# Kernel tuning notes

Hardware: AMD Instinct MI355X
Metric: run time of the kernel (lower is better)

Reference implementation:

```python
import jax, jax.numpy as jnp
import numpy as np

B, N, C, H = 4, 4096, 1024, 16
D = C // H


def setup_inputs() -> dict:
    key = jax.random.key(0)
    ks = jax.random.split(key, 15)
    s = 0.02
    f = lambda k, shp: jax.random.normal(k, shp, dtype=jnp.float32) * s
    return {
        "x": f(ks[0], (B, N, C)),
        "qkv_w": f(ks[1], (C, 3 * C)),
        "qkv_b": f(ks[2], (3 * C,)),
        "out_w": f(ks[3], (C, C)),
        "out_b": f(ks[4], (C,)),
        # NB: original code dynamically re-creates position_bias as (1, N, H, H)
        # because q/k/v are never transposed to (B,H,N,D); attention runs over heads.
        "pos_bias": f(ks[5], (1, N, H, H)),
        "conv_w": f(ks[6], (C, C)),
        "conv_b": f(ks[7], (C,)),
        "pw_w": f(ks[8], (C, C, 1)),   # Conv1d kernel_size=1: (out, in, k)
        "pw_b": f(ks[9], (C,)),
        "dw_w": f(ks[10], (C, 1, 3)),  # depthwise Conv1d groups=C: (out, in/groups=1, k)
        "dw_b": f(ks[11], (C,)),
        "tok_w": f(ks[12], (C, C)),
        "tok_b": f(ks[13], (C,)),
    }


def reference(x, qkv_w, qkv_b, out_w, out_b, pos_bias,
              conv_w, conv_b, pw_w, pw_b, dw_w, dw_b, tok_w, tok_b):
    b, n, c = x.shape
    h = pos_bias.shape[2]
    d = c // h
    scale = d ** (-0.5)

    # ---- attention branch (faithful to source: heads axis is attended over) ----
    qkv = (x @ qkv_w + qkv_b).reshape(b, n, h, 3 * d)
    q, k, v = jnp.split(qkv, 3, axis=-1)  # each (B, N, H, D)
    scores = jnp.einsum("bnhd,bngd->bnhg", q, k) * scale + pos_bias  # (B, N, H, H)
    attn_w = jax.nn.softmax(scores, axis=-1)
    attn = jnp.einsum("bnhg,bngd->bnhd", attn_w, v).reshape(b, n, c)
    attn = attn @ out_w + out_b

    # ---- convolutional branch ----
    xc = x @ conv_w + conv_b            # (B, N, C)
    xc = xc.transpose(0, 2, 1)          # (B, C, N)
    dn = ("NCH", "OIH", "NCH")
    xc = jax.lax.conv_general_dilated(xc, pw_w, (1,), [(0, 0)],
                                      dimension_numbers=dn) + pw_b[None, :, None]
    xc = jax.lax.conv_general_dilated(xc, dw_w, (1,), [(1, 1)],
                                      dimension_numbers=dn,
                                      feature_group_count=c) + dw_b[None, :, None]
    xc = xc.transpose(0, 2, 1) @ tok_w + tok_b  # (B, N, C)

    return attn + xc
```

## Files before the change

kernel.cpp:

```cpp
#include <hip/hip_runtime.h>
#include <hip/hip_bf16.h>


typedef __attribute__((ext_vector_type(8))) short sh8;
typedef __attribute__((ext_vector_type(4))) float f4;

__device__ __forceinline__ float bf2f(short s) {
  unsigned u = ((unsigned)(unsigned short)s) << 16;
  return __builtin_bit_cast(float, u);
}
__device__ __forceinline__ short f2bf(float f) {
  return __builtin_bit_cast(short, __float2bfloat16(f));
}
__device__ __forceinline__ void g2l16(const void* g, void* l) {
  __builtin_amdgcn_global_load_lds(
      (const __attribute__((address_space(1))) unsigned int*)g,
      (__attribute__((address_space(3))) unsigned int*)l, 16, 0, 0);
}

__global__ __launch_bounds__(256) void cvt_f32_bf16(
    const float* __restrict__ src, short* __restrict__ dst, int n8) {
  int i = blockIdx.x * 256 + threadIdx.x;
  if (i >= n8) return;
  float4 a = ((const float4*)src)[i * 2];
  float4 b = ((const float4*)src)[i * 2 + 1];
  sh8 o;
  o[0] = f2bf(a.x); o[1] = f2bf(a.y); o[2] = f2bf(a.z); o[3] = f2bf(a.w);
  o[4] = f2bf(b.x); o[5] = f2bf(b.y); o[6] = f2bf(b.z); o[7] = f2bf(b.w);
  ((sh8*)dst)[i] = o;
}

__global__ __launch_bounds__(256) void transpose_f32_bf16(
    const float* __restrict__ src, short* __restrict__ dst,
    int N, int ldd, int coff) {
  __shared__ float tile[32][33];
  int kb = blockIdx.y * 32, nb = blockIdx.x * 32;
  int tx = threadIdx.x, ty = threadIdx.y;
#pragma unroll
  for (int j = 0; j < 32; j += 8)
    tile[ty + j][tx] = src[(size_t)(kb + ty + j) * N + nb + tx];
  __syncthreads();
#pragma unroll
  for (int j = 0; j < 32; j += 8)
    dst[(size_t)(nb + ty + j) * ldd + coff + kb + tx] = f2bf(tile[tx][ty + j]);
}

__global__ __launch_bounds__(256) void prep_misc(
    const float* __restrict__ pw_w, const float* __restrict__ conv_b,
    const float* __restrict__ pw_b, const float* __restrict__ qkv_b,
    const float* __restrict__ out_b, const float* __restrict__ tok_b,
    const float* __restrict__ dw_w, const float* __restrict__ dw_b,
    float* __restrict__ bias4, float* __restrict__ bcat,
    float* __restrict__ dw0, float* __restrict__ dw1,
    float* __restrict__ dw2, float* __restrict__ dwb) {
  int o = blockIdx.x;
  if (o < 1024) {
    float part = 0.f;
    for (int i = threadIdx.x; i < 1024; i += 256)
      part += pw_w[(size_t)o * 1024 + i] * conv_b[i];
#pragma unroll
    for (int off = 32; off >= 1; off >>= 1) part += __shfl_down(part, off);
    __shared__ float red[4];
    int wid = threadIdx.x >> 6, lane = threadIdx.x & 63;
    if (lane == 0) red[wid] = part;
    __syncthreads();
    if (threadIdx.x == 0) {
      float s = red[0] + red[1] + red[2] + red[3];
      bias4[3072 + o] = s + pw_b[o];
      bcat[o] = out_b[o] + tok_b[o];
      dw0[o] = dw_w[o * 3 + 0];
      dw1[o] = dw_w[o * 3 + 1];
      dw2[o] = dw_w[o * 3 + 2];
      dwb[o] = dw_b[o];
    }
  }
  if (threadIdx.x == 0) bias4[o] = qkv_b[o];
}

template <int OUT_BF16>
__global__ __launch_bounds__(256, 2) void gemm128(
    const short* __restrict__ A, const short* __restrict__ Bt,
    void* __restrict__ Cp, const float* __restrict__ bias, int K, int ldc) {
  __shared__ short As[128 * 32];
  __shared__ short Bs[128 * 32];
  const int wid = threadIdx.x >> 6, lane = threadIdx.x & 63;
  const int bm = blockIdx.y, bn = blockIdx.x;
  const int wr = wid >> 1, wc = wid & 1;
  const size_t abase = (size_t)bm * 128 * K;
  const size_t bbase = (size_t)bn * 128 * K;
  const int r16 = lane & 15, ko = (lane >> 4) * 8;

  f4 acc[4][4] = {};

  for (int k0 = 0; k0 < K; k0 += 32) {
    __syncthreads();
#pragma unroll
    for (int c = 0; c < 2; ++c) {
      int ch = c * 256 + wid * 64 + lane;
      int row = ch >> 2, kc = (ch & 3) * 8;
      g2l16(A + abase + (size_t)row * K + k0 + kc, &As[ch * 8]);
      g2l16(Bt + bbase + (size_t)row * K + k0 + kc, &Bs[ch * 8]);
    }
    __syncthreads();
    sh8 af[4], bf[4];
#pragma unroll
    for (int i = 0; i < 4; ++i)
      af[i] = *(const sh8*)&As[(wr * 64 + i * 16 + r16) * 32 + ko];
#pragma unroll
    for (int j = 0; j < 4; ++j)
      bf[j] = *(const sh8*)&Bs[(wc * 64 + j * 16 + r16) * 32 + ko];
#pragma unroll
    for (int i = 0; i < 4; ++i)
#pragma unroll
      for (int j = 0; j < 4; ++j)
        acc[i][j] = __builtin_amdgcn_mfma_f32_16x16x32_bf16(af[i], bf[j],
                                                            acc[i][j], 0, 0, 0);
  }

  const int crow = wr * 64 + (lane >> 4) * 4;
  const int ccol = wc * 64 + r16;
#pragma unroll
  for (int i = 0; i < 4; ++i) {
#pragma unroll
    for (int j = 0; j < 4; ++j) {
      int col = bn * 128 + ccol + j * 16;
      float bv = bias ? bias[col] : 0.f;
#pragma unroll
      for (int r = 0; r < 4; ++r) {
        int row = bm * 128 + crow + i * 16 + r;
        float v = acc[i][j][r] + bv;
        if (OUT_BF16)
          ((short*)Cp)[(size_t)row * ldc + col] = f2bf(v);
        else
          ((float*)Cp)[(size_t)row * ldc + col] = v;
      }
    }
  }
}

template <int OUT_BF16>
__global__ __launch_bounds__(512, 2) void gemm256(
    const short* __restrict__ A, const short* __restrict__ Bt,
    void* __restrict__ Cp, const float* __restrict__ bias,
    int K, int ldc, int nbn) {
  __shared__ short lds[65536];
  const int tid = threadIdx.x;
  const int lane = tid & 63, wid = tid >> 6;
  const int wr = wid >> 2, wc = wid & 3;
  const int r16 = lane & 15;
  const int kidx = ((lane >> 4) ^ ((r16 >> 1) & 3)) << 3;

  const int cpx = gridDim.x >> 3;
  const int swz = (blockIdx.x & 7) * cpx + (blockIdx.x >> 3);
  const int bm = swz / nbn, bn = swz % nbn;

  const short* Ag = A + (size_t)bm * 256 * K;
  const short* Bg = Bt + (size_t)bn * 256 * K;

  int goff0, goff1, loff0, loff1;
  {
    int s0 = tid, row0 = s0 >> 2;
    int kc0 = (s0 & 3) ^ ((row0 >> 1) & 3);
    goff0 = row0 * K + kc0 * 8;
    loff0 = s0 * 8;
    int s1 = 512 + tid, row1 = s1 >> 2;
    int kc1 = (s1 & 3) ^ ((row1 >> 1) & 3);
    goff1 = row1 * K + kc1 * 8;
    loff1 = s1 * 8;
  }

  f4 acc[8][4] = {};
  const int NT = K >> 5;

#define STAGE_FULL(KT, B)                                   \
  do {                                                      \
    short* lb = &lds[(B) * 16384];                          \
    const short* ga = Ag + (KT) * 32;                       \
    const short* gb = Bg + (KT) * 32;                       \
    g2l16(ga + goff0, lb + loff0);                          \
    g2l16(gb + goff0, lb + 8192 + loff0);                   \
    g2l16(ga + goff1, lb + loff1);                          \
    g2l16(gb + goff1, lb + 8192 + loff1);                   \
  } while (0)

  STAGE_FULL(0, 0);
  STAGE_FULL(1, 1);
  asm volatile("s_waitcnt vmcnt(4)" ::: "memory");
  __builtin_amdgcn_sched_barrier(0);
  __builtin_amdgcn_s_barrier();
  __builtin_amdgcn_sched_barrier(0);

  for (int t = 0; t < NT; ++t) {
    const short* Ab = &lds[(t & 3) * 16384];
    const short* Bb = Ab + 8192;
    const int kt2 = (t + 2 < NT) ? t + 2 : 0;
    STAGE_FULL(kt2, (t + 2) & 3);

    sh8 af[8], bfr[4];
#pragma unroll
    for (int i = 0; i < 4; ++i)
      af[i] = *(const sh8*)&Ab[(wr * 128 + i * 16 + r16) * 32 + kidx];
#pragma unroll
    for (int j = 0; j < 4; ++j)
      bfr[j] = *(const sh8*)&Bb[(wc * 64 + j * 16 + r16) * 32 + kidx];
#pragma unroll
    for (int i = 4; i < 8; ++i)
      af[i] = *(const sh8*)&Ab[(wr * 128 + i * 16 + r16) * 32 + kidx];

    __builtin_amdgcn_s_setprio(1);
#pragma unroll
    for (int i = 0; i < 8; ++i)
#pragma unroll
      for (int j = 0; j < 4; ++j)
        acc[i][j] = __builtin_amdgcn_mfma_f32_16x16x32_bf16(af[i], bfr[j],
                                                            acc[i][j], 0, 0, 0);
    __builtin_amdgcn_s_setprio(0);
    __builtin_amdgcn_sched_barrier(0);
    asm volatile("s_waitcnt vmcnt(4)" ::: "memory");
    __builtin_amdgcn_sched_barrier(0);
    __builtin_amdgcn_s_barrier();
    __builtin_amdgcn_sched_barrier(0);
  }
#undef STAGE_FULL

  const int crow0 = bm * 256 + wr * 128 + (lane >> 4) * 4;
  const int ccol0 = bn * 256 + wc * 64 + r16;
  float bv[4];
#pragma unroll
  for (int j = 0; j < 4; ++j) bv[j] = bias ? bias[ccol0 + j * 16] : 0.f;
#pragma unroll
  for (int i = 0; i < 8; ++i) {
#pragma unroll
    for (int r = 0; r < 4; ++r) {
      size_t rowoff = (size_t)(crow0 + i * 16 + r) * ldc + ccol0;
#pragma unroll
      for (int j = 0; j < 4; ++j) {
        float v = acc[i][j][r] + bv[j];
        if (OUT_BF16)
          ((short*)Cp)[rowoff + j * 16] = f2bf(v);
        else
          ((float*)Cp)[rowoff + j * 16] = v;
      }
    }
  }
}

__global__ __launch_bounds__(256) void attn_fused(
    const short* __restrict__ qkvx, const float* __restrict__ pos_bias,
    short* __restrict__ xcat) {
  __shared__ short sq[4 * 3072];
  int t0 = blockIdx.x * 4;
#pragma unroll
  for (int c = 0; c < 6; ++c) {
    int g = c * 256 + threadIdx.x;
    int tok = (g * 683) >> 18;
    int off = g - tok * 384;
    ((sh8*)sq)[tok * 384 + off] =
        *(const sh8*)(qkvx + (size_t)(t0 + tok) * 4096 + off * 8);
  }
  __syncthreads();

  int wid = threadIdx.x >> 6, lane = threadIdx.x & 63;
  int t = t0 + wid, n = t & 4095;
  int h = lane >> 2, sub = lane & 3;
  const short* base = sq + wid * 3072 + h * 192;

  float qf[64];
#pragma unroll
  for (int c = 0; c < 8; ++c) {
    sh8 v8 = *(const sh8*)(base + c * 8);
#pragma unroll
    for (int j = 0; j < 8; ++j) qf[c * 8 + j] = bf2f(v8[j]);
  }

  const float* pb = pos_bias + (size_t)n * 256 + h * 16 + sub * 4;
  float p[4];
  float m = -1e30f;
#pragma unroll
  for (int g4 = 0; g4 < 4; ++g4) {
    int g = sub * 4 + g4;
    const short* kk = sq + wid * 3072 + g * 192 + 64;
    float acc = 0.f;
#pragma unroll
    for (int c = 0; c < 8; ++c) {
      sh8 k8 = *(const sh8*)(kk + c * 8);
#pragma unroll
      for (int j = 0; j < 8; ++j) acc += qf[c * 8 + j] * bf2f(k8[j]);
    }
    p[g4] = acc * 0.125f + pb[g4];
    m = fmaxf(m, p[g4]);
  }
  m = fmaxf(m, __shfl_xor(m, 1));
  m = fmaxf(m, __shfl_xor(m, 2));
  float sum = 0.f;
#pragma unroll
  for (int g4 = 0; g4 < 4; ++g4) {
    p[g4] = __expf(p[g4] - m);
    sum += p[g4];
  }
  sum += __shfl_xor(sum, 1);
  sum += __shfl_xor(sum, 2);
  float inv = 1.0f / sum;
#pragma unroll
  for (int g4 = 0; g4 < 4; ++g4) p[g4] *= inv;

  float pall[16];
#pragma unroll
  for (int g = 0; g < 16; ++g)
    pall[g] = __shfl(p[g & 3], (lane & 60) | (g >> 2));

  float o[16] = {};
#pragma unroll
  for (int g = 0; g < 16; ++g) {
    const short* vv = sq + wid * 3072 + g * 192 + 128 + sub * 16;
    sh8 va = *(const sh8*)vv;
    sh8 vb = *(const sh8*)(vv + 8);
#pragma unroll
    for (int j = 0; j < 8; ++j) {
      o[j] += pall[g] * bf2f(va[j]);
      o[8 + j] += pall[g] * bf2f(vb[j]);
    }
  }
  sh8 oa, ob;
#pragma unroll
  for (int j = 0; j < 8; ++j) {
    oa[j] = f2bf(o[j]);
    ob[j] = f2bf(o[8 + j]);
  }
  short* dst = xcat + (size_t)t * 2048 + h * 64 + sub * 16;
  *(sh8*)dst = oa;
  *(sh8*)(dst + 8) = ob;
}

__global__ __launch_bounds__(256) void dwconv(
    const short* __restrict__ qkvx, const float* __restrict__ dw0,
    const float* __restrict__ dw1, const float* __restrict__ dw2,
    const float* __restrict__ dwb, short* __restrict__ xcat) {
  int idx = blockIdx.x * 256 + threadIdx.x;
  int t = idx >> 7, c = (idx & 127) * 8;
  int n = t & 4095;
  const short* row = qkvx + (size_t)t * 4096 + 3072 + c;
  sh8 mid = *(const sh8*)row;
  sh8 lo = {}, hi = {};
  if (n > 0) lo = *(const sh8*)(row - 4096);
  if (n < 4095) hi = *(const sh8*)(row + 4096);
  sh8 out;
#pragma unroll
  for (int j = 0; j < 8; ++j) {
    float v = dw0[c + j] * bf2f(lo[j]) + dw1[c + j] * bf2f(mid[j]) +
              dw2[c + j] * bf2f(hi[j]) + dwb[c + j];
    out[j] = f2bf(v);
  }
  *(sh8*)(xcat + (size_t)t * 2048 + 1024 + c) = out;
}

extern "C" void kernel_launch(void* const* d_in, const int* in_sizes, int n_in,
                              void* d_out, int out_size, void* d_ws,
                              size_t ws_size, hipStream_t stream) {
  const float* x      = (const float*)d_in[0];
  const float* qkv_w  = (const float*)d_in[1];
  const float* qkv_b  = (const float*)d_in[2];
  const float* out_w  = (const float*)d_in[3];
  const float* out_b  = (const float*)d_in[4];
  const float* pos_b  = (const float*)d_in[5];
  const float* conv_w = (const float*)d_in[6];
  const float* conv_b = (const float*)d_in[7];
  const float* pw_w   = (const float*)d_in[8];
  const float* pw_b   = (const float*)d_in[9];
  const float* dw_w   = (const float*)d_in[10];
  const float* dw_b   = (const float*)d_in[11];
  const float* tok_w  = (const float*)d_in[12];
  const float* tok_b  = (const float*)d_in[13];

  const int M = 16384;
  char* ws = (char*)d_ws;
  size_t off = 0;
  auto alloc = [&](size_t bytes) -> void* {
    void* p = ws + off;
    off += (bytes + 255) & ~(size_t)255;
    return p;
  };
  short* xb    = (short*)alloc((size_t)M * 1024 * 2);
  short* wbig  = (short*)alloc((size_t)4096 * 1024 * 2);
  short* wcatT = (short*)alloc((size_t)1024 * 2048 * 2);
  short* convb = (short*)alloc((size_t)1024 * 1024 * 2);
  short* pwb   = (short*)alloc((size_t)1024 * 1024 * 2);
  short* qkvx  = (short*)alloc((size_t)M * 4096 * 2);
  short* xcat  = (short*)alloc((size_t)M * 2048 * 2);
  float* bias4 = (float*)alloc(4096 * 4);
  float* bcat  = (float*)alloc(1024 * 4);
  float* dw0   = (float*)alloc(1024 * 4);
  float* dw1   = (float*)alloc(1024 * 4);
  float* dw2   = (float*)alloc(1024 * 4);
  float* dwb   = (float*)alloc(1024 * 4);
  (void)ws_size; (void)in_sizes; (void)n_in; (void)out_size;

  cvt_f32_bf16<<<8192, 256, 0, stream>>>(x, xb, M * 1024 / 8);
  cvt_f32_bf16<<<512, 256, 0, stream>>>(conv_w, convb, 1024 * 1024 / 8);
  cvt_f32_bf16<<<512, 256, 0, stream>>>(pw_w, pwb, 1024 * 1024 / 8);
  transpose_f32_bf16<<<dim3(96, 32), dim3(32, 8), 0, stream>>>(qkv_w, wbig, 3072, 1024, 0);
  transpose_f32_bf16<<<dim3(32, 32), dim3(32, 8), 0, stream>>>(out_w, wcatT, 1024, 2048, 0);
  transpose_f32_bf16<<<dim3(32, 32), dim3(32, 8), 0, stream>>>(tok_w, wcatT, 1024, 2048, 1024);
  prep_misc<<<3072, 256, 0, stream>>>(pw_w, conv_b, pw_b, qkv_b, out_b, tok_b,
                                      dw_w, dw_b, bias4, bcat, dw0, dw1, dw2, dwb);
  gemm128<1><<<dim3(8, 8), 256, 0, stream>>>(pwb, convb, wbig + (size_t)3072 * 1024,
                                             nullptr, 1024, 1024);

  gemm256<1><<<1024, 512, 0, stream>>>(xb, wbig, qkvx, bias4, 1024, 4096, 16);

  attn_fused<<<4096, 256, 0, stream>>>(qkvx, pos_b, xcat);
  dwconv<<<8192, 256, 0, stream>>>(qkvx, dw0, dw1, dw2, dwb, xcat);

  gemm256<0><<<256, 512, 0, stream>>>(xcat, wcatT, d_out, bcat, 2048, 1024, 4);
}
```

Before: 338.4 us.

## Double-buffer LDS fragments in registers and deepen global prefetch to three stages

Restructures the GEMM main loop to load the next k-tile's LDS fragments into a second register set while MFMAs run on the current set, unrolling the loop by two. Global-to-LDS prefetch distance grows from two to three tiles within the 4-buffer ring. This aims to hide LDS read latency behind MFMA work, at the cost of roughly doubling fragment registers (possible occupancy or spill pressure). It assumes NT is even, and the waitcnt/barrier accounting must stay valid with the deeper prefetch.

```diff
diff --git a/kernel.cpp b/kernel.cpp
--- a/kernel.cpp
+++ b/kernel.cpp
@@ -183,45 +183,71 @@
     g2l16(gb + goff1, lb + 8192 + loff1);                   \
   } while (0)
 
+#define LOADFRAG(AF, BF, BUFIDX)                                          \
+  do {                                                                    \
+    const short* Ab_ = &lds[(BUFIDX) * 16384];                            \
+    const short* Bb_ = Ab_ + 8192;                                        \
+    _Pragma("unroll")                                                     \
+    for (int i = 0; i < 8; ++i)                                           \
+      AF[i] = *(const sh8*)&Ab_[(wr * 128 + i * 16 + r16) * 32 + kidx];   \
+    _Pragma("unroll")                                                     \
+    for (int j = 0; j < 4; ++j)                                           \
+      BF[j] = *(const sh8*)&Bb_[(wc * 64 + j * 16 + r16) * 32 + kidx];    \
+  } while (0)
+
+#define MFMA_ALL(AF, BF)                                                  \
+  do {                                                                    \
+    _Pragma("unroll")                                                     \
+    for (int i = 0; i < 8; ++i)                                           \
+      _Pragma("unroll")                                                   \
+      for (int j = 0; j < 4; ++j)                                         \
+        acc[i][j] = __builtin_amdgcn_mfma_f32_16x16x32_bf16(              \
+            AF[i], BF[j], acc[i][j], 0, 0, 0);                            \
+  } while (0)
+
   STAGE_FULL(0, 0);
   STAGE_FULL(1, 1);
+  STAGE_FULL(2, 2);
   asm volatile("s_waitcnt vmcnt(4)" ::: "memory");
   __builtin_amdgcn_sched_barrier(0);
   __builtin_amdgcn_s_barrier();
   __builtin_amdgcn_sched_barrier(0);
 
-  for (int t = 0; t < NT; ++t) {
-    const short* Ab = &lds[(t & 3) * 16384];
-    const short* Bb = Ab + 8192;
-    const int kt2 = (t + 2 < NT) ? t + 2 : 0;
-    STAGE_FULL(kt2, (t + 2) & 3);
-
-    sh8 af[8], bfr[4];
-#pragma unroll
-    for (int i = 0; i < 4; ++i)
-      af[i] = *(const sh8*)&Ab[(wr * 128 + i * 16 + r16) * 32 + kidx];
-#pragma unroll
-    for (int j = 0; j < 4; ++j)
-      bfr[j] = *(const sh8*)&Bb[(wc * 64 + j * 16 + r16) * 32 + kidx];
-#pragma unroll
-    for (int i = 4; i < 8; ++i)
-      af[i] = *(const sh8*)&Ab[(wr * 128 + i * 16 + r16) * 32 + kidx];
-
+  sh8 afA[8], bfA[4], afB[8], bfB[4];
+  LOADFRAG(afA, bfA, 0);
+
+  for (int t = 0; t < NT; t += 2) {
+    LOADFRAG(afB, bfB, (t + 1) & 3);
+    {
+      const int kt = (t + 3 < NT) ? t + 3 : 0;
+      STAGE_FULL(kt, (t + 3) & 3);
+    }
     __builtin_amdgcn_s_setprio(1);
-#pragma unroll
-    for (int i = 0; i < 8; ++i)
-#pragma unroll
-      for (int j = 0; j < 4; ++j)
-        acc[i][j] = __builtin_amdgcn_mfma_f32_16x16x32_bf16(af[i], bfr[j],
-                                                            acc[i][j], 0, 0, 0);
+    MFMA_ALL(afA, bfA);
     __builtin_amdgcn_s_setprio(0);
     __builtin_amdgcn_sched_barrier(0);
     asm volatile("s_waitcnt vmcnt(4)" ::: "memory");
     __builtin_amdgcn_sched_barrier(0);
     __builtin_amdgcn_s_barrier();
     __builtin_amdgcn_sched_barrier(0);
+
+    LOADFRAG(afA, bfA, (t + 2) & 3);
+    {
+      const int kt = (t + 4 < NT) ? t + 4 : 0;
+      STAGE_FULL(kt, (t + 4) & 3);
+    }
+    __builtin_amdgcn_s_setprio(1);
+    MFMA_ALL(afB, bfB);
+    __builtin_amdgcn_s_setprio(0);
+    __builtin_amdgcn_sched_barrier(0);
+    asm volatile("s_waitcnt vmcnt(4)" ::: "memory");
+    __builtin_amdgcn_sched_barrier(0);
+    __builtin_amdgcn_s_barrier();
+    __builtin_amdgcn_sched_barrier(0);
   }
 #undef STAGE_FULL
+#undef LOADFRAG
+#undef MFMA_ALL
 
   const int crow0 = bm * 256 + wr * 128 + (lane >> 4) * 4;
   const int ccol0 = bn * 256 + wc * 64 + r16;
```

After: 330.4 us. -2.4%, faster.

## Switch GEMM mainloop to double-buffered 64-wide K steps with full sync

Applied to the files above, without the earlier changes.

Restructures the bf16 GEMM main loop from a 4-slot ring of 32-wide K tiles, prefetched two tiles ahead, to a 2-slot double buffer holding 64-wide K tiles, prefetched one tile ahead. Each iteration now runs two MFMA sub-steps, which halves the number of barriers per K. The fine-grained vmcnt(4) wait is replaced by __syncthreads, which waits for all outstanding loads, including the prefetch just issued. That likely serializes load latency with compute and reduces overlap.

```diff
diff --git a/kernel.cpp b/kernel.cpp
--- a/kernel.cpp
+++ b/kernel.cpp
@@ -170,43 +170,39 @@
   }
 
   f4 acc[8][4] = {};
-  const int NT = K >> 5;
-
-#define STAGE_FULL(KT, B)                                   \
+  const int NT = K >> 6;
+
+#define STAGE8(KT, BUF)                                     \
   do {                                                      \
-    short* lb = &lds[(B) * 16384];                          \
-    const short* ga = Ag + (KT) * 32;                       \
-    const short* gb = Bg + (KT) * 32;                       \
-    g2l16(ga + goff0, lb + loff0);                          \
-    g2l16(gb + goff0, lb + 8192 + loff0);                   \
-    g2l16(ga + goff1, lb + loff1);                          \
-    g2l16(gb + goff1, lb + 8192 + loff1);                   \
+    short* lb = &lds[(BUF) * 32768];                        \
+    const short* ga0 = Ag + (KT) * 64;                      \
+    const short* gb0 = Bg + (KT) * 64;                      \
+    g2l16(ga0 + goff0, lb + loff0);                         \
+    g2l16(gb0 + goff0, lb + 8192 + loff0);                  \
+    g2l16(ga0 + goff1, lb + loff1);                         \
+    g2l16(gb0 + goff1, lb + 8192 + loff1);                  \
+    g2l16(ga0 + 32 + goff0, lb + 16384 + loff0);            \
+    g2l16(gb0 + 32 + goff0, lb + 24576 + loff0);            \
+    g2l16(ga0 + 32 + goff1, lb + 16384 + loff1);            \
+    g2l16(gb0 + 32 + goff1, lb + 24576 + loff1);            \
   } while (0)
 
-  STAGE_FULL(0, 0);
-  STAGE_FULL(1, 1);
-  asm volatile("s_waitcnt vmcnt(4)" ::: "memory");
-  __builtin_amdgcn_sched_barrier(0);
-  __builtin_amdgcn_s_barrier();
-  __builtin_amdgcn_sched_barrier(0);
+  STAGE8(0, 0);
+  __syncthreads();
 
   for (int t = 0; t < NT; ++t) {
-    const short* Ab = &lds[(t & 3) * 16384];
-    const short* Bb = Ab + 8192;
-    const int kt2 = (t + 2 < NT) ? t + 2 : 0;
-    STAGE_FULL(kt2, (t + 2) & 3);
-
+    const int kt = (t + 1 < NT) ? t + 1 : 0;
+    STAGE8(kt, (t + 1) & 1);
+
+    const short* base = &lds[(t & 1) * 32768];
     sh8 af[8], bfr[4];
-#pragma unroll
-    for (int i = 0; i < 4; ++i)
-      af[i] = *(const sh8*)&Ab[(wr * 128 + i * 16 + r16) * 32 + kidx];
+
+#pragma unroll
+    for (int i = 0; i < 8; ++i)
+      af[i] = *(const sh8*)&base[(wr * 128 + i * 16 + r16) * 32 + kidx];
 #pragma unroll
     for (int j = 0; j < 4; ++j)
-      bfr[j] = *(const sh8*)&Bb[(wc * 64 + j * 16 + r16) * 32 + kidx];
-#pragma unroll
-    for (int i = 4; i < 8; ++i)
-      af[i] = *(const sh8*)&Ab[(wr * 128 + i * 16 + r16) * 32 + kidx];
-
+      bfr[j] = *(const sh8*)&base[8192 + (wc * 64 + j * 16 + r16) * 32 + kidx];
     __builtin_amdgcn_s_setprio(1);
 #pragma unroll
     for (int i = 0; i < 8; ++i)
@@ -215,13 +211,27 @@
         acc[i][j] = __builtin_amdgcn_mfma_f32_16x16x32_bf16(af[i], bfr[j],
                                                             acc[i][j], 0, 0, 0);
     __builtin_amdgcn_s_setprio(0);
+
+#pragma unroll
+    for (int i = 0; i < 8; ++i)
+      af[i] = *(const sh8*)&base[16384 + (wr * 128 + i * 16 + r16) * 32 + kidx];
+#pragma unroll
+    for (int j = 0; j < 4; ++j)
+      bfr[j] = *(const sh8*)&base[24576 + (wc * 64 + j * 16 + r16) * 32 + kidx];
+    __builtin_amdgcn_s_setprio(1);
+#pragma unroll
+    for (int i = 0; i < 8; ++i)
+#pragma unroll
+      for (int j = 0; j < 4; ++j)
+        acc[i][j] = __builtin_amdgcn_mfma_f32_16x16x32_bf16(af[i], bfr[j],
+                                                            acc[i][j], 0, 0, 0);
+    __builtin_amdgcn_s_setprio(0);
+
     __builtin_amdgcn_sched_barrier(0);
-    asm volatile("s_waitcnt vmcnt(4)" ::: "memory");
+    __syncthreads();
     __builtin_amdgcn_sched_barrier(0);
-    __builtin_amdgcn_s_barrier();
-    __builtin_amdgcn_sched_barrier(0);
-  }
-#undef STAGE_FULL
+  }
+#undef STAGE8
 
   const int crow0 = bm * 256 + wr * 128 + (lane >> 4) * 4;
   const int ccol0 = bn * 256 + wc * 64 + r16;
```

Result: no change. 334.9 us (-1.0%).

## Shrink GEMM tile to 128x256 with triple-buffered LDS and fuse dwconv into attention

Applied to the files above, without the earlier changes.

The main GEMM tile drops from 256x256 to 128x256 and the LDS ring goes from four buffers to three. This halves the accumulator registers and LDS use so the launch bound can request 4 blocks per SM, and it doubles the grid for both GEMMs to improve occupancy and wave balance. The depthwise conv is folded into the attention kernel: each block loads a 6-row slice of the conv channels into LDS, which removes a separate launch and reads neighbour rows once per block. The risk is lower per-block data reuse in the GEMM, which means more global/L2 traffic per FLOP. It also puts extra LDS pressure on the fused kernel.

```diff
diff --git a/kernel.cpp b/kernel.cpp
--- a/kernel.cpp
+++ b/kernel.cpp
@@ -139,11 +139,11 @@
 }
 
 template <int OUT_BF16>
-__global__ __launch_bounds__(512, 2) void gemm256(
+__global__ __launch_bounds__(512, 4) void gemmMain(
     const short* __restrict__ A, const short* __restrict__ Bt,
     void* __restrict__ Cp, const float* __restrict__ bias,
     int K, int ldc, int nbn) {
-  __shared__ short lds[65536];
+  __shared__ short lds[36864];
   const int tid = threadIdx.x;
   const int lane = tid & 63, wid = tid >> 6;
   const int wr = wid >> 2, wc = wid & 3;
@@ -154,82 +154,84 @@
   const int swz = (blockIdx.x & 7) * cpx + (blockIdx.x >> 3);
   const int bm = swz / nbn, bn = swz % nbn;
 
-  const short* Ag = A + (size_t)bm * 256 * K;
+  const short* Ag = A + (size_t)bm * 128 * K;
   const short* Bg = Bt + (size_t)bn * 256 * K;
 
-  int goff0, goff1, loff0, loff1;
+  int gA, lA, gB0, lB0, gB1, lB1;
   {
-    int s0 = tid, row0 = s0 >> 2;
-    int kc0 = (s0 & 3) ^ ((row0 >> 1) & 3);
-    goff0 = row0 * K + kc0 * 8;
-    loff0 = s0 * 8;
-    int s1 = 512 + tid, row1 = s1 >> 2;
-    int kc1 = (s1 & 3) ^ ((row1 >> 1) & 3);
-    goff1 = row1 * K + kc1 * 8;
-    loff1 = s1 * 8;
-  }
-
-  f4 acc[8][4] = {};
+    int ch = tid, row = ch >> 2;
+    int kc = (ch & 3) ^ ((row >> 1) & 3);
+    gA = row * K + kc * 8;
+    lA = ch * 8;
+    int c0 = tid, r0 = c0 >> 2;
+    int k0 = (c0 & 3) ^ ((r0 >> 1) & 3);
+    gB0 = r0 * K + k0 * 8;
+    lB0 = 4096 + c0 * 8;
+    int c1 = 512 + tid, r1 = c1 >> 2;
+    int k1 = (c1 & 3) ^ ((r1 >> 1) & 3);
+    gB1 = r1 * K + k1 * 8;
+    lB1 = 4096 + c1 * 8;
+  }
+
+  f4 acc[4][4] = {};
   const int NT = K >> 5;
 
-#define STAGE_FULL(KT, B)                                   \
+#define STAGE3(KT, BUF)                                     \
   do {                                                      \
-    short* lb = &lds[(B) * 16384];                          \
+    short* lb = &lds[(BUF) * 12288];                        \
     const short* ga = Ag + (KT) * 32;                       \
     const short* gb = Bg + (KT) * 32;                       \
-    g2l16(ga + goff0, lb + loff0);                          \
-    g2l16(gb + goff0, lb + 8192 + loff0);                   \
-    g2l16(ga + goff1, lb + loff1);                          \
-    g2l16(gb + goff1, lb + 8192 + loff1);                   \
+    g2l16(ga + gA, lb + lA);                                \
+    g2l16(gb + gB0, lb + lB0);                              \
+    g2l16(gb + gB1, lb + lB1);                              \
   } while (0)
 
-  STAGE_FULL(0, 0);
-  STAGE_FULL(1, 1);
-  asm volatile("s_waitcnt vmcnt(4)" ::: "memory");
+  STAGE3(0, 0);
+  STAGE3(1, 1);
+  asm volatile("s_waitcnt vmcnt(3)" ::: "memory");
   __builtin_amdgcn_sched_barrier(0);
   __builtin_amdgcn_s_barrier();
   __builtin_amdgcn_sched_barrier(0);
 
+  int cb = 0;
   for (int t = 0; t < NT; ++t) {
-    const short* Ab = &lds[(t & 3) * 16384];
-    const short* Bb = Ab + 8192;
-    const int kt2 = (t + 2 < NT) ? t + 2 : 0;
-    STAGE_FULL(kt2, (t + 2) & 3);
-
-    sh8 af[8], bfr[4];
+    int sb = cb + 2; if (sb >= 3) sb -= 3;
+    const int kt = (t + 2 < NT) ? t + 2 : 0;
+    STAGE3(kt, sb);
+
+    const short* base = &lds[cb * 12288];
+    sh8 af[4], bfr[4];
 #pragma unroll
     for (int i = 0; i < 4; ++i)
-      af[i] = *(const sh8*)&Ab[(wr * 128 + i * 16 + r16) * 32 + kidx];
+      af[i] = *(const sh8*)&base[(wr * 64 + i * 16 + r16) * 32 + kidx];
 #pragma unroll
     for (int j = 0; j < 4; ++j)
-      bfr[j] = *(const sh8*)&Bb[(wc * 64 + j * 16 + r16) * 32 + kidx];
-#pragma unroll
-    for (int i = 4; i < 8; ++i)
-      af[i] = *(const sh8*)&Ab[(wr * 128 + i * 16 + r16) * 32 + kidx];
+      bfr[j] = *(const sh8*)&base[4096 + (wc * 64 + j * 16 + r16) * 32 + kidx];
 
     __builtin_amdgcn_s_setprio(1);
 #pragma unroll
-    for (int i = 0; i < 8; ++i)
+    for (int i = 0; i < 4; ++i)
 #pragma unroll
       for (int j = 0; j < 4; ++j)
         acc[i][j] = __builtin_amdgcn_mfma_f32_16x16x32_bf16(af[i], bfr[j],
                                                             acc[i][j], 0, 0, 0);
     __builtin_amdgcn_s_setprio(0);
     __builtin_amdgcn_sched_barrier(0);
-    asm volatile("s_waitcnt vmcnt(4)" ::: "memory");
+    asm volatile("s_waitcnt vmcnt(3)" ::: "memory");
     __builtin_amdgcn_sched_barrier(0);
     __builtin_amdgcn_s_barrier();
     __builtin_amdgcn_sched_barrier(0);
-  }
-#undef STAGE_FULL
-
-  const int crow0 = bm * 256 + wr * 128 + (lane >> 4) * 4;
+    cb = cb + 1; if (cb >= 3) cb -= 3;
+  }
+#undef STAGE3
+
+  const int crow0 = bm * 128 + wr * 64 + (lane >> 4) * 4;
   const int ccol0 = bn * 256 + wc * 64 + r16;
   float bv[4];
 #pragma unroll
   for (int j = 0; j < 4; ++j) bv[j] = bias ? bias[ccol0 + j * 16] : 0.f;
 #pragma unroll
-  for (int i = 0; i < 8; ++i) {
+  for (int i = 0; i < 4; ++i) {
 #pragma unroll
     for (int r = 0; r < 4; ++r) {
       size_t rowoff = (size_t)(crow0 + i * 16 + r) * ldc + ccol0;
@@ -245,10 +247,13 @@
   }
 }
 
-__global__ __launch_bounds__(256) void attn_fused(
+__global__ __launch_bounds__(256) void epilogue(
     const short* __restrict__ qkvx, const float* __restrict__ pos_bias,
+    const float* __restrict__ dw0, const float* __restrict__ dw1,
+    const float* __restrict__ dw2, const float* __restrict__ dwb,
     short* __restrict__ xcat) {
   __shared__ short sq[4 * 3072];
+  __shared__ short slice[6 * 1024];
   int t0 = blockIdx.x * 4;
 #pragma unroll
   for (int c = 0; c < 6; ++c) {
@@ -258,6 +263,16 @@
     ((sh8*)sq)[tok * 384 + off] =
         *(const sh8*)(qkvx + (size_t)(t0 + tok) * 4096 + off * 8);
   }
+#pragma unroll
+  for (int s = 0; s < 3; ++s) {
+    int g = s * 256 + threadIdx.x;
+    int r = g >> 7, off = g & 127;
+    int gr = t0 - 1 + r;
+    sh8 v = {};
+    if (gr >= 0 && gr < 16384)
+      v = *(const sh8*)(qkvx + (size_t)gr * 4096 + 3072 + off * 8);
+    ((sh8*)slice)[g] = v;
+  }
   __syncthreads();
 
   int wid = threadIdx.x >> 6, lane = threadIdx.x & 63;
@@ -330,28 +345,27 @@
   short* dst = xcat + (size_t)t * 2048 + h * 64 + sub * 16;
   *(sh8*)dst = oa;
   *(sh8*)(dst + 8) = ob;
-}
-
-__global__ __launch_bounds__(256) void dwconv(
-    const short* __restrict__ qkvx, const float* __restrict__ dw0,
-    const float* __restrict__ dw1, const float* __restrict__ dw2,
-    const float* __restrict__ dwb, short* __restrict__ xcat) {
-  int idx = blockIdx.x * 256 + threadIdx.x;
-  int t = idx >> 7, c = (idx & 127) * 8;
-  int n = t & 4095;
-  const short* row = qkvx + (size_t)t * 4096 + 3072 + c;
-  sh8 mid = *(const sh8*)row;
-  sh8 lo = {}, hi = {};
-  if (n > 0) lo = *(const sh8*)(row - 4096);
-  if (n < 4095) hi = *(const sh8*)(row + 4096);
-  sh8 out;
-#pragma unroll
-  for (int j = 0; j < 8; ++j) {
-    float v = dw0[c + j] * bf2f(lo[j]) + dw1[c + j] * bf2f(mid[j]) +
-              dw2[c + j] * bf2f(hi[j]) + dwb[c + j];
-    out[j] = f2bf(v);
-  }
-  *(sh8*)(xcat + (size_t)t * 2048 + 1024 + c) = out;
+
+#pragma unroll
+  for (int it = 0; it < 2; ++it) {
+    int w = it * 256 + threadIdx.x;
+    int tok = w >> 7, co = (w & 127) * 8;
+    int tt = t0 + tok, nn = tt & 4095;
+    const short* lo8 = slice + tok * 1024 + co;
+    const short* mi8 = lo8 + 1024;
+    const short* hi8 = lo8 + 2048;
+    sh8 lo = (nn > 0) ? *(const sh8*)lo8 : sh8{};
+    sh8 mi = *(const sh8*)mi8;
+    sh8 hi = (nn < 4095) ? *(const sh8*)hi8 : sh8{};
+    sh8 out;
+#pragma unroll
+    for (int j = 0; j < 8; ++j) {
+      float v = dw0[co + j] * bf2f(lo[j]) + dw1[co + j] * bf2f(mi[j]) +
+                dw2[co + j] * bf2f(hi[j]) + dwb[co + j];
+      out[j] = f2bf(v);
+    }
+    *(sh8*)(xcat + (size_t)tt * 2048 + 1024 + co) = out;
+  }
 }
 
 extern "C" void kernel_launch(void* const* d_in, const int* in_sizes, int n_in,
@@ -406,10 +420,9 @@
   gemm128<1><<<dim3(8, 8), 256, 0, stream>>>(pwb, convb, wbig + (size_t)3072 * 1024,
                                              nullptr, 1024, 1024);
 
-  gemm256<1><<<1024, 512, 0, stream>>>(xb, wbig, qkvx, bias4, 1024, 4096, 16);
-
-  attn_fused<<<4096, 256, 0, stream>>>(qkvx, pos_b, xcat);
-  dwconv<<<8192, 256, 0, stream>>>(qkvx, dw0, dw1, dw2, dwb, xcat);
-
-  gemm256<0><<<256, 512, 0, stream>>>(xcat, wcatT, d_out, bcat, 2048, 1024, 4);
-}
+  gemmMain<1><<<2048, 512, 0, stream>>>(xb, wbig, qkvx, bias4, 1024, 4096, 16);
+
+  epilogue<<<4096, 256, 0, stream>>>(qkvx, pos_b, dw0, dw1, dw2, dwb, xcat);
+
+  gemmMain<0><<<512, 512, 0, stream>>>(xcat, wcatT, d_out, bcat, 2048, 1024, 4);
+}
```

Measured after the change: 347.3 us. 2.6% more time.
